# Kernel tuning notes

Hardware: AMD Instinct MI355X
Metric: run time of the kernel (lower is better)

## Reference

```python
import jax, jax.numpy as jnp
import numpy as np

B, S, D = 4, 1024, 1024
H, DK, DV = 16, 64, 64
EPS = 1e-5

def setup_inputs() -> dict:
    key = jax.random.key(0)
    ks = jax.random.split(key, 13)
    sc = lambda n: 1.0 / np.sqrt(n)
    return {
        "Q": jax.random.normal(ks[0], (B, S, D), jnp.float32),
        "K": jax.random.normal(ks[1], (B, S, D), jnp.float32),
        "V": jax.random.normal(ks[2], (B, S, D), jnp.float32),
        "Wq": jax.random.normal(ks[3], (D, H * DK), jnp.float32) * sc(D),
        "bq": jax.random.normal(ks[4], (H * DK,), jnp.float32) * 0.01,
        "Wk": jax.random.normal(ks[5], (D, H * DK), jnp.float32) * sc(D),
        "bk": jax.random.normal(ks[6], (H * DK,), jnp.float32) * 0.01,
        "Wv": jax.random.normal(ks[7], (D, H * DV), jnp.float32) * sc(D),
        "bv": jax.random.normal(ks[8], (H * DV,), jnp.float32) * 0.01,
        "Wo": jax.random.normal(ks[9], (H * DV, D), jnp.float32) * sc(H * DV),
        "bo": jax.random.normal(ks[10], (D,), jnp.float32) * 0.01,
        "pos_k": jax.random.normal(ks[11], (H * S, DK), jnp.float32) * 0.02,
        "pos_v": jax.random.normal(ks[12], (H * S, DV), jnp.float32) * 0.02,
        "gamma": jnp.ones((D,), jnp.float32),
        "beta": jnp.zeros((D,), jnp.float32),
    }

def reference(Q, K, V, Wq, bq, Wk, bk, Wv, bv, Wo, bo, pos_k, pos_v, gamma, beta):
    b = Q.shape[0]
    # projections + head split: [b, h, s, dk/dv]
    q = (Q @ Wq + bq).reshape(b, S, H, DK).transpose(0, 2, 1, 3)
    k = (K @ Wk + bk).reshape(b, S, H, DK).transpose(0, 2, 1, 3)
    v = (V @ Wv + bv).reshape(b, S, H, DV).transpose(0, 2, 1, 3)
    # pos_ids = arange(H*S).view(1, H, S) -> embedding lookup is just a reshape
    K_pos = pos_k.reshape(1, H, S, DK)
    V_pos = pos_v.reshape(1, H, S, DV)
    scores = jnp.einsum("bhqd,bhkd->bhqk", q, k + K_pos) / np.sqrt(DK).astype(np.float32)
    attn = jax.nn.softmax(scores, axis=-1)
    context = jnp.einsum("bhqk,bhkd->bhqd", attn, v + V_pos)
    context = context.transpose(0, 2, 1, 3).reshape(b, S, H * DV)
    out = context @ Wo + bo + Q  # residual
    mu = jnp.mean(out, axis=-1, keepdims=True)
    var = jnp.var(out, axis=-1, keepdims=True)
    out = (out - mu) * jax.lax.rsqrt(var + EPS) * gamma + beta
    return (out, attn)
```

## Files before the change

kernel.cpp:

```cpp
#include <hip/hip_runtime.h>
#include <cstdint>
#include <cstddef>


typedef __attribute__((ext_vector_type(8))) short short8;
typedef __attribute__((ext_vector_type(4))) short short4v;
typedef __attribute__((ext_vector_type(4))) float f32x4;

typedef __attribute__((address_space(1))) void gl_void;
typedef __attribute__((address_space(3))) void lds_void;

#define MFMA16(a, b, c) __builtin_amdgcn_mfma_f32_16x16x32_bf16(a, b, c, 0, 0, 0)
#define GLL(src, dst) __builtin_amdgcn_global_load_lds((gl_void*)(src), (lds_void*)(dst), 16, 0, 0)
#define SBAR() __builtin_amdgcn_s_barrier()
#define WAIT_VM(n) asm volatile("s_waitcnt vmcnt(" #n ")" ::: "memory")

__device__ __forceinline__ unsigned short f2bf(float f) {
  union { float f; unsigned u; } v; v.f = f;
  unsigned r = v.u + 0x7FFFu + ((v.u >> 16) & 1u);
  return (unsigned short)(r >> 16);
}
__device__ __forceinline__ float bf2f(unsigned short h) {
  union { unsigned u; float f; } v; v.u = ((unsigned)h) << 16;
  return v.f;
}

__global__ __launch_bounds__(256) void transpose_w(
    const float* __restrict__ wq, const float* __restrict__ wk,
    const float* __restrict__ wv, const float* __restrict__ wo,
    unsigned short* __restrict__ wt) {
  __shared__ unsigned short tile[64][68];
  const int z = blockIdx.z;
  const float* W = (z == 0) ? wq : (z == 1) ? wk : (z == 2) ? wv : wo;
  unsigned short* out = wt + (size_t)z * 1048576;
  const int n0 = blockIdx.x * 64, k0 = blockIdx.y * 64;
  const int tr = threadIdx.x >> 4;
  const int tc = (threadIdx.x & 15) * 4;
#pragma unroll
  for (int i = 0; i < 4; ++i) {
    int k = tr + i * 16;
    float4 x = *reinterpret_cast<const float4*>(W + (size_t)(k0 + k) * 1024 + n0 + tc);
    tile[k][tc + 0] = f2bf(x.x); tile[k][tc + 1] = f2bf(x.y);
    tile[k][tc + 2] = f2bf(x.z); tile[k][tc + 3] = f2bf(x.w);
  }
  __syncthreads();
#pragma unroll
  for (int i = 0; i < 4; ++i) {
    int n = tr + i * 16;
    short4v o;
    o[0] = (short)tile[tc + 0][n]; o[1] = (short)tile[tc + 1][n];
    o[2] = (short)tile[tc + 2][n]; o[3] = (short)tile[tc + 3][n];
    *reinterpret_cast<short4v*>(out + (size_t)(n0 + n) * 1024 + k0 + tc) = o;
  }
}

__global__ __launch_bounds__(256) void gemm_qkv(
    const float* __restrict__ Qf, const float* __restrict__ Kf,
    const float* __restrict__ Vf, const unsigned short* __restrict__ wt,
    const float* __restrict__ bq, const float* __restrict__ bk,
    const float* __restrict__ bv, const float* __restrict__ pos_k,
    const float* __restrict__ pos_v, unsigned short* __restrict__ qb,
    unsigned short* __restrict__ kbuf, unsigned short* __restrict__ vT) {
  __shared__ unsigned short lds[16384];
  const int z = blockIdx.z;
  const float* A = (z == 0) ? Qf : (z == 1) ? Kf : Vf;
  const unsigned short* Bt = wt + (size_t)z * 1048576;
  const float* bias = (z == 0) ? bq : (z == 1) ? bk : bv;

  const int tid = threadIdx.x;
  const int lane = tid & 63;
  const int w = tid >> 6;
  const int g = lane >> 4;
  const int lr = lane & 15;
  const int wg = blockIdx.y * 8 + blockIdx.x;
  const int lg = (wg & 7) * 32 + (wg >> 3);
  const int m0 = (lg >> 3) << 7;
  const int n0 = (lg & 7) << 7;
  const int wm = w >> 1, wn = w & 1;

  const int ra0 = tid >> 2, ca = tid & 3;
  const int ra1 = ra0 + 64;
  const int wA0 = ra0 * 64 + ((ca ^ ((ra0 >> 1) & 3)) << 4);
  const int wA1 = ra1 * 64 + ((ca ^ ((ra1 >> 1) & 3)) << 4);
  const float* a0p = A + (size_t)(m0 + ra0) * 1024 + ca * 8;
  const float* a1p = A + (size_t)(m0 + ra1) * 1024 + ca * 8;

  const int c0 = (w << 6) + lane;
  const int r0 = c0 >> 2;
  const int sl0 = (c0 & 3) ^ ((r0 >> 1) & 3);
  const int c1 = c0 + 256;
  const int r1 = c1 >> 2;
  const int sl1 = (c1 & 3) ^ ((r1 >> 1) & 3);
  const size_t gb0 = ((size_t)(n0 + r0) << 10) + (sl0 << 3);
  const size_t gb1 = ((size_t)(n0 + r1) << 10) + (sl1 << 3);
  char* ldsc = (char*)lds;

  int offA[4], offB[4];
#pragma unroll
  for (int i = 0; i < 4; ++i) {
    int rt = (wm << 6) + (i << 4) + lr;
    offA[i] = rt * 64 + ((g ^ ((rt >> 1) & 3)) << 4);
    int nt = (wn << 6) + (i << 4) + lr;
    offB[i] = nt * 64 + ((g ^ ((nt >> 1) & 3)) << 4);
  }

  f32x4 acc[4][4] = {};

  {
    const float4 fa = *reinterpret_cast<const float4*>(a0p);
    const float4 fb = *reinterpret_cast<const float4*>(a0p + 4);
    const float4 fc = *reinterpret_cast<const float4*>(a1p);
    const float4 fd = *reinterpret_cast<const float4*>(a1p + 4);
    short8 pa, pb;
    pa[0] = (short)f2bf(fa.x); pa[1] = (short)f2bf(fa.y);
    pa[2] = (short)f2bf(fa.z); pa[3] = (short)f2bf(fa.w);
    pa[4] = (short)f2bf(fb.x); pa[5] = (short)f2bf(fb.y);
    pa[6] = (short)f2bf(fb.z); pa[7] = (short)f2bf(fb.w);
    pb[0] = (short)f2bf(fc.x); pb[1] = (short)f2bf(fc.y);
    pb[2] = (short)f2bf(fc.z); pb[3] = (short)f2bf(fc.w);
    pb[4] = (short)f2bf(fd.x); pb[5] = (short)f2bf(fd.y);
    pb[6] = (short)f2bf(fd.z); pb[7] = (short)f2bf(fd.w);
    *reinterpret_cast<short8*>(ldsc + wA0) = pa;
    *reinterpret_cast<short8*>(ldsc + wA1) = pb;
    __builtin_amdgcn_global_load_lds((gl_void*)(Bt + gb0),
                                     (lds_void*)(ldsc + 16384 + (w << 10)), 16, 0, 0);
    __builtin_amdgcn_global_load_lds((gl_void*)(Bt + gb1),
                                     (lds_void*)(ldsc + 16384 + 4096 + (w << 10)), 16, 0, 0);
    __syncthreads();
  }

  for (int kt = 0; kt < 32; ++kt) {
    const int cur = (kt & 1) << 13;
    const int nxt = ((kt + 1) & 1) << 13;
    float4 fa, fb, fc, fd;
    if (kt < 31) {
      const int kb32 = (kt + 1) << 5;
      __builtin_amdgcn_global_load_lds((gl_void*)(Bt + gb0 + kb32),
                                       (lds_void*)(ldsc + 16384 + nxt + (w << 10)), 16, 0, 0);
      __builtin_amdgcn_global_load_lds((gl_void*)(Bt + gb1 + kb32),
                                       (lds_void*)(ldsc + 16384 + nxt + 4096 + (w << 10)), 16, 0, 0);
      fa = *reinterpret_cast<const float4*>(a0p + kb32);
      fb = *reinterpret_cast<const float4*>(a0p + kb32 + 4);
      fc = *reinterpret_cast<const float4*>(a1p + kb32);
      fd = *reinterpret_cast<const float4*>(a1p + kb32 + 4);
    }
    short8 am[4], bn[4];
#pragma unroll
    for (int i = 0; i < 4; ++i) {
      am[i] = *reinterpret_cast<const short8*>(ldsc + cur + offA[i]);
      bn[i] = *reinterpret_cast<const short8*>(ldsc + 16384 + cur + offB[i]);
    }
#pragma unroll
    for (int i = 0; i < 4; ++i)
#pragma unroll
      for (int j = 0; j < 4; ++j)
        acc[i][j] = MFMA16(am[i], bn[j], acc[i][j]);
    if (kt < 31) {
      short8 pa, pb;
      pa[0] = (short)f2bf(fa.x); pa[1] = (short)f2bf(fa.y);
      pa[2] = (short)f2bf(fa.z); pa[3] = (short)f2bf(fa.w);
      pa[4] = (short)f2bf(fb.x); pa[5] = (short)f2bf(fb.y);
      pa[6] = (short)f2bf(fb.z); pa[7] = (short)f2bf(fb.w);
      pb[0] = (short)f2bf(fc.x); pb[1] = (short)f2bf(fc.y);
      pb[2] = (short)f2bf(fc.z); pb[3] = (short)f2bf(fc.w);
      pb[4] = (short)f2bf(fd.x); pb[5] = (short)f2bf(fd.y);
      pb[6] = (short)f2bf(fd.z); pb[7] = (short)f2bf(fd.w);
      *reinterpret_cast<short8*>(ldsc + nxt + wA0) = pa;
      *reinterpret_cast<short8*>(ldsc + nxt + wA1) = pb;
    }
    __syncthreads();
  }

#pragma unroll
  for (int i = 0; i < 4; ++i) {
#pragma unroll
    for (int j = 0; j < 4; ++j) {
      const int n = n0 + (wn << 6) + (j << 4) + lr;
      const int hh = n >> 6, dk = n & 63;
      const float bs = bias[n];
      const int mb = m0 + (wm << 6) + (i << 4) + (g << 2);
      const int b = mb >> 10, s0 = mb & 1023;
      if (z == 2) {
        short4v o;
#pragma unroll
        for (int r = 0; r < 4; ++r) {
          const float val = acc[i][j][r] + bs +
                            pos_v[((((size_t)hh << 10) + s0 + r) << 6) + dk];
          o[r] = (short)f2bf(val);
        }
        *reinterpret_cast<short4v*>(
            vT + ((size_t)((b * 16 + hh) * 64 + dk) << 10) + s0) = o;
      } else {
#pragma unroll
        for (int r = 0; r < 4; ++r) {
          float val = acc[i][j][r];
          if (z == 0) {
            val = (val + bs) * 0.180336880111f;
          } else {
            val = val + bs + pos_k[((((size_t)hh << 10) + s0 + r) << 6) + dk];
          }
          unsigned short* dst = (z == 0) ? qb : kbuf;
          dst[((((size_t)(b * 16 + hh) << 10) + s0 + r) << 6) + dk] = f2bf(val);
        }
      }
    }
  }
}

__global__ __launch_bounds__(256) void attn_fused(
    const unsigned short* __restrict__ qb,
    const unsigned short* __restrict__ kb,
    const unsigned short* __restrict__ vT,
    unsigned short* __restrict__ ctxb,
    float* __restrict__ attn_out) {
  __shared__ char smem[40960];
  const int tid = threadIdx.x;
  const int lane = tid & 63;
  const int w = tid >> 6;
  const int g = lane >> 4;
  const int lr = lane & 15;
  const int wg = ((blockIdx.x & 7) << 7) + (blockIdx.x >> 3);
  const int bh = wg >> 4, qt = wg & 15;
  const int b = bh >> 4, h = bh & 15;
  const int qrow0 = (qt << 6) + (w << 4);
  const size_t headoff = (size_t)bh << 16;

  const size_t qoff = headoff + (size_t)(qrow0 + lr) * 64 + (g << 3);
  const short8 a0 = *reinterpret_cast<const short8*>(qb + qoff);
  const short8 a1 = *reinterpret_cast<const short8*>(qb + qoff + 32);

  const int key0 = tid >> 3, sl0 = (tid & 7) ^ (key0 & 7);
  const int key1 = 32 + (tid >> 3), sl1 = (tid & 7) ^ (key1 & 7);
  const unsigned short* ks0 = kb + headoff + (size_t)key0 * 64 + (sl0 << 3);
  const unsigned short* ks1 = kb + headoff + (size_t)key1 * 64 + (sl1 << 3);
  const unsigned short* vs0 = vT + headoff + ((size_t)key0 << 10) + (sl0 << 3);
  const unsigned short* vs1 = vT + headoff + ((size_t)key1 << 10) + (sl1 << 3);

  GLL(ks0, smem + (w << 10));
  GLL(ks1, smem + 4096 + (w << 10));
  GLL(ks0 + 4096, smem + 8192 + (w << 10));
  GLL(ks1 + 4096, smem + 8192 + 4096 + (w << 10));

  float l[4] = {0.f, 0.f, 0.f, 0.f};
  for (int ct = 0; ct < 16; ++ct) {
    if (ct < 15) WAIT_VM(2); else WAIT_VM(0);
    SBAR();
    const char* kl = smem + ((ct & 1) << 13);
#pragma unroll
    for (int kf = 0; kf < 4; ++kf) {
      const int kr = (kf << 4) + lr;
      const char* row = kl + (kr << 7);
      const short8 b0 = *reinterpret_cast<const short8*>(row + ((g ^ (kr & 7)) << 4));
      const short8 b1 = *reinterpret_cast<const short8*>(row + (((4 + g) ^ (kr & 7)) << 4));
      f32x4 acc = {0.f, 0.f, 0.f, 0.f};
      acc = MFMA16(a0, b0, acc);
      acc = MFMA16(a1, b1, acc);
#pragma unroll
      for (int r = 0; r < 4; ++r) l[r] += exp2f(acc[r]);
    }
    SBAR();
    if (ct + 2 < 16) {
      const int koff = (ct + 2) << 12;
      const int bo = (ct & 1) << 13;
      GLL(ks0 + koff, smem + bo + (w << 10));
      GLL(ks1 + koff, smem + bo + 4096 + (w << 10));
    }
  }
#pragma unroll
  for (int r = 0; r < 4; ++r) {
    l[r] += __shfl_xor(l[r], 1);
    l[r] += __shfl_xor(l[r], 2);
    l[r] += __shfl_xor(l[r], 4);
    l[r] += __shfl_xor(l[r], 8);
  }
  float inv[4];
#pragma unroll
  for (int r = 0; r < 4; ++r) inv[r] = 1.0f / l[r];

  GLL(ks0, smem + (w << 10));
  GLL(ks1, smem + 4096 + (w << 10));
  GLL(vs0, smem + 16384 + (w << 10));
  GLL(vs1, smem + 16384 + 4096 + (w << 10));
  GLL(ks0 + 4096, smem + 8192 + (w << 10));
  GLL(ks1 + 4096, smem + 8192 + 4096 + (w << 10));
  GLL(vs0 + 64, smem + 16384 + 8192 + (w << 10));
  GLL(vs1 + 64, smem + 16384 + 8192 + 4096 + (w << 10));

  char* ew = smem + 32768 + (w << 11);
  float* ab = attn_out + ((size_t)bh << 20);
  f32x4 ctx[4] = {};

  for (int ct = 0; ct < 16; ++ct) {
    if (ct == 0) { WAIT_VM(4); }
    else if (ct == 15) { WAIT_VM(4); }
    else { WAIT_VM(8); }
    SBAR();
    const int cur = (ct & 1) << 13;
    const int kc0 = ct << 6;
    const char* kl = smem + cur;
    const char* vl = smem + 16384 + cur;

#pragma unroll
    for (int kf = 0; kf < 4; ++kf) {
      const int kr = (kf << 4) + lr;
      const char* row = kl + (kr << 7);
      const short8 b0 = *reinterpret_cast<const short8*>(row + ((g ^ (kr & 7)) << 4));
      const short8 b1 = *reinterpret_cast<const short8*>(row + (((4 + g) ^ (kr & 7)) << 4));
      f32x4 acc = {0.f, 0.f, 0.f, 0.f};
      acc = MFMA16(a0, b0, acc);
      acc = MFMA16(a1, b1, acc);
#pragma unroll
      for (int r = 0; r < 4; ++r) {
        const float p = exp2f(acc[r]) * inv[r];
        const int prow = (g << 2) + r;
        const int kc = (kf << 4) + lr;
        *(unsigned short*)(ew + (prow << 7) + ((((kc >> 3) ^ (prow & 7))) << 4) +
                           ((kc & 7) << 1)) = f2bf(p);
      }
    }

#pragma unroll
    for (int p2 = 0; p2 < 2; ++p2) {
      const int row = lane >> 2;
      const int s = (lane & 3) + (p2 << 2);
      const short8 pv = *reinterpret_cast<const short8*>(
          ew + (row << 7) + ((s ^ (row & 7)) << 4));
      float* dst = ab + ((size_t)(qrow0 + row) << 10) + kc0 + (s << 3);
      float4 o0, o1;
      o0.x = bf2f((unsigned short)pv[0]); o0.y = bf2f((unsigned short)pv[1]);
      o0.z = bf2f((unsigned short)pv[2]); o0.w = bf2f((unsigned short)pv[3]);
      o1.x = bf2f((unsigned short)pv[4]); o1.y = bf2f((unsigned short)pv[5]);
      o1.z = bf2f((unsigned short)pv[6]); o1.w = bf2f((unsigned short)pv[7]);
      *reinterpret_cast<float4*>(dst) = o0;
      *reinterpret_cast<float4*>(dst + 4) = o1;
    }

    const short8 pa0 = *reinterpret_cast<const short8*>(
        ew + (lr << 7) + ((g ^ (lr & 7)) << 4));
    const short8 pa1 = *reinterpret_cast<const short8*>(
        ew + (lr << 7) + (((4 + g) ^ (lr & 7)) << 4));
#pragma unroll
    for (int dt = 0; dt < 4; ++dt) {
      const int dv = (dt << 4) + lr;
      const char* vrow = vl + (dv << 7);
      const short8 v0 = *reinterpret_cast<const short8*>(vrow + ((g ^ (dv & 7)) << 4));
      const short8 v1 = *reinterpret_cast<const short8*>(vrow + (((4 + g) ^ (dv & 7)) << 4));
      ctx[dt] = MFMA16(pa0, v0, ctx[dt]);
      ctx[dt] = MFMA16(pa1, v1, ctx[dt]);
    }
    SBAR();
    if (ct + 2 < 16) {
      const int kn = (ct + 2) << 6;
      const int bo = (ct & 1) << 13;
      GLL(ks0 + ((size_t)kn << 6), smem + bo + (w << 10));
      GLL(ks1 + ((size_t)kn << 6), smem + bo + 4096 + (w << 10));
      GLL(vs0 + kn, smem + 16384 + bo + (w << 10));
      GLL(vs1 + kn, smem + 16384 + bo + 4096 + (w << 10));
    }
  }

#pragma unroll
  for (int dt = 0; dt < 4; ++dt) {
#pragma unroll
    for (int r = 0; r < 4; ++r) {
      const int srow = qrow0 + (g << 2) + r;
      const int n = (h << 6) + (dt << 4) + lr;
      ctxb[((((size_t)(b << 10)) + srow) << 10) + n] = f2bf(ctx[dt][r]);
    }
  }
}

__global__ __launch_bounds__(256) void gemm_out(
    const unsigned short* __restrict__ A, const unsigned short* __restrict__ Bt,
    const float* __restrict__ bias, const float* __restrict__ resid,
    float* __restrict__ outf) {
  __shared__ unsigned short lds[16384];
  const int tid = threadIdx.x;
  const int lane = tid & 63;
  const int w = tid >> 6;
  const int g = lane >> 4;
  const int lr = lane & 15;
  const int wg = blockIdx.y * 8 + blockIdx.x;
  const int lg = (wg & 7) * 32 + (wg >> 3);
  const int m0 = (lg >> 3) << 7;
  const int n0 = (lg & 7) << 7;
  const int wm = w >> 1, wn = w & 1;

  const int c0 = (w << 6) + lane;
  const int r0 = c0 >> 2;
  const int sl0 = (c0 & 3) ^ ((r0 >> 1) & 3);
  const int c1 = c0 + 256;
  const int r1 = c1 >> 2;
  const int sl1 = (c1 & 3) ^ ((r1 >> 1) & 3);

  const size_t ga0 = ((size_t)(m0 + r0) << 10) + (sl0 << 3);
  const size_t ga1 = ((size_t)(m0 + r1) << 10) + (sl1 << 3);
  const size_t gb0 = ((size_t)(n0 + r0) << 10) + (sl0 << 3);
  const size_t gb1 = ((size_t)(n0 + r1) << 10) + (sl1 << 3);

  char* ldsc = (char*)lds;

  int offA[4], offB[4];
#pragma unroll
  for (int i = 0; i < 4; ++i) {
    int rt = (wm << 6) + (i << 4) + lr;
    offA[i] = rt * 64 + ((g ^ ((rt >> 1) & 3)) << 4);
    int nt = (wn << 6) + (i << 4) + lr;
    offB[i] = nt * 64 + ((g ^ ((nt >> 1) & 3)) << 4);
  }

  __builtin_amdgcn_global_load_lds((gl_void*)(A + ga0),
                                   (lds_void*)(ldsc + (w << 10)), 16, 0, 0);
  __builtin_amdgcn_global_load_lds((gl_void*)(A + ga1),
                                   (lds_void*)(ldsc + 4096 + (w << 10)), 16, 0, 0);
  __builtin_amdgcn_global_load_lds((gl_void*)(Bt + gb0),
                                   (lds_void*)(ldsc + 16384 + (w << 10)), 16, 0, 0);
  __builtin_amdgcn_global_load_lds((gl_void*)(Bt + gb1),
                                   (lds_void*)(ldsc + 16384 + 4096 + (w << 10)), 16, 0, 0);
  __syncthreads();

  f32x4 acc[4][4] = {};
  for (int kt = 0; kt < 32; ++kt) {
    const int cur = (kt & 1) << 13;
    if (kt < 31) {
      const int nxt = ((kt + 1) & 1) << 13;
      const int kb32 = (kt + 1) << 5;
      __builtin_amdgcn_global_load_lds((gl_void*)(A + ga0 + kb32),
                                       (lds_void*)(ldsc + nxt + (w << 10)), 16, 0, 0);
      __builtin_amdgcn_global_load_lds((gl_void*)(A + ga1 + kb32),
                                       (lds_void*)(ldsc + nxt + 4096 + (w << 10)), 16, 0, 0);
      __builtin_amdgcn_global_load_lds((gl_void*)(Bt + gb0 + kb32),
                                       (lds_void*)(ldsc + 16384 + nxt + (w << 10)), 16, 0, 0);
      __builtin_amdgcn_global_load_lds((gl_void*)(Bt + gb1 + kb32),
                                       (lds_void*)(ldsc + 16384 + nxt + 4096 + (w << 10)), 16, 0, 0);
    }
    short8 am[4], bn[4];
#pragma unroll
    for (int i = 0; i < 4; ++i) {
      am[i] = *reinterpret_cast<const short8*>(ldsc + cur + offA[i]);
      bn[i] = *reinterpret_cast<const short8*>(ldsc + 16384 + cur + offB[i]);
    }
#pragma unroll
    for (int i = 0; i < 4; ++i)
#pragma unroll
      for (int j = 0; j < 4; ++j)
        acc[i][j] = MFMA16(am[i], bn[j], acc[i][j]);
    __syncthreads();
  }

#pragma unroll
  for (int i = 0; i < 4; ++i) {
#pragma unroll
    for (int j = 0; j < 4; ++j) {
      const int n = n0 + (wn << 6) + (j << 4) + lr;
      const float bs = bias[n];
#pragma unroll
      for (int r = 0; r < 4; ++r) {
        const int m = m0 + (wm << 6) + (i << 4) + (g << 2) + r;
        outf[((size_t)m << 10) + n] =
            acc[i][j][r] + bs + resid[((size_t)m << 10) + n];
      }
    }
  }
}

__global__ __launch_bounds__(256) void layernorm_kernel(
    const float* __restrict__ x, const float* __restrict__ gamma,
    const float* __restrict__ beta, float* __restrict__ out) {
  __shared__ float red[8];
  const int row = blockIdx.x, t = threadIdx.x;
  const float4 v = *reinterpret_cast<const float4*>(x + ((size_t)row << 10) + t * 4);
  float s1 = v.x + v.y + v.z + v.w;
  float s2 = v.x * v.x + v.y * v.y + v.z * v.z + v.w * v.w;
#pragma unroll
  for (int off = 1; off < 64; off <<= 1) {
    s1 += __shfl_xor(s1, off);
    s2 += __shfl_xor(s2, off);
  }
  const int w = t >> 6;
  if ((t & 63) == 0) { red[w * 2] = s1; red[w * 2 + 1] = s2; }
  __syncthreads();
  s1 = red[0] + red[2] + red[4] + red[6];
  s2 = red[1] + red[3] + red[5] + red[7];
  const float mu = s1 * (1.0f / 1024.0f);
  const float var = s2 * (1.0f / 1024.0f) - mu * mu;
  const float rs = rsqrtf(var + 1e-5f);
  const float4 gm = *reinterpret_cast<const float4*>(gamma + t * 4);
  const float4 bt = *reinterpret_cast<const float4*>(beta + t * 4);
  float4 o;
  o.x = (v.x - mu) * rs * gm.x + bt.x;
  o.y = (v.y - mu) * rs * gm.y + bt.y;
  o.z = (v.z - mu) * rs * gm.z + bt.z;
  o.w = (v.w - mu) * rs * gm.w + bt.w;
  *reinterpret_cast<float4*>(out + ((size_t)row << 10) + t * 4) = o;
}

static constexpr size_t OFF_QB = 0;
static constexpr size_t OFF_KB = 8388608;
static constexpr size_t OFF_VT = 16777216;
static constexpr size_t OFF_WT = 25165824;
static constexpr size_t OFF_CTX = 33554432;
static constexpr size_t OFF_LN = 41943040;

extern "C" void kernel_launch(void* const* d_in, const int* in_sizes, int n_in,
                              void* d_out, int out_size, void* d_ws, size_t ws_size,
                              hipStream_t stream) {
  (void)in_sizes; (void)n_in; (void)out_size; (void)ws_size;
  const float* Q = (const float*)d_in[0];
  const float* K = (const float*)d_in[1];
  const float* V = (const float*)d_in[2];
  const float* Wq = (const float*)d_in[3];
  const float* bq = (const float*)d_in[4];
  const float* Wk = (const float*)d_in[5];
  const float* bk = (const float*)d_in[6];
  const float* Wv = (const float*)d_in[7];
  const float* bv = (const float*)d_in[8];
  const float* Wo = (const float*)d_in[9];
  const float* bo = (const float*)d_in[10];
  const float* pos_k = (const float*)d_in[11];
  const float* pos_v = (const float*)d_in[12];
  const float* gamma = (const float*)d_in[13];
  const float* beta = (const float*)d_in[14];

  char* ws = (char*)d_ws;
  unsigned short* qb = (unsigned short*)(ws + OFF_QB);
  unsigned short* kb = (unsigned short*)(ws + OFF_KB);
  unsigned short* vT = (unsigned short*)(ws + OFF_VT);
  unsigned short* wt = (unsigned short*)(ws + OFF_WT);
  unsigned short* ctxb = (unsigned short*)(ws + OFF_CTX);
  float* lnb = (float*)(ws + OFF_LN);

  float* outF = (float*)d_out;
  float* attnF = outF + 4194304;

  transpose_w<<<dim3(16, 16, 4), 256, 0, stream>>>(Wq, Wk, Wv, Wo, wt);
  gemm_qkv<<<dim3(8, 32, 3), 256, 0, stream>>>(Q, K, V, wt, bq, bk, bv,
                                               pos_k, pos_v, qb, kb, vT);
  attn_fused<<<dim3(1024), 256, 0, stream>>>(qb, kb, vT, ctxb, attnF);
  gemm_out<<<dim3(8, 32), 256, 0, stream>>>(ctxb, wt + 3145728, bo, Q, lnb);
  layernorm_kernel<<<4096, 256, 0, stream>>>(lnb, gamma, beta, outF);
}
```

Baseline: 198.4 us.

## Double attention block size to 128 queries and pipeline gemm_out loads two stages ahead

The attention kernel now runs 512 threads per block covering 128 query rows, so each K/V tile staged in LDS is reused by eight waves instead of four. With eight waves, each thread issues one tile load instead of two, and the LDS footprint grows to make room for the extra per-wave softmax scratch. Separately, gemm_out switches from one-step prefetch with __syncthreads to a two-deep global_load_lds pipeline with explicit vmcnt waits and barriers. Risks are lower occupancy and fewer blocks per CU for attention, and a correctness dependency on the hand-counted vmcnt values.

```diff
diff --git a/kernel.cpp b/kernel.cpp
--- a/kernel.cpp
+++ b/kernel.cpp
@@ -207,22 +207,22 @@
   }
 }
 
-__global__ __launch_bounds__(256) void attn_fused(
+__global__ __launch_bounds__(512) void attn_fused(
     const unsigned short* __restrict__ qb,
     const unsigned short* __restrict__ kb,
     const unsigned short* __restrict__ vT,
     unsigned short* __restrict__ ctxb,
     float* __restrict__ attn_out) {
-  __shared__ char smem[40960];
+  __shared__ char smem[49152];
   const int tid = threadIdx.x;
   const int lane = tid & 63;
   const int w = tid >> 6;
   const int g = lane >> 4;
   const int lr = lane & 15;
-  const int wg = ((blockIdx.x & 7) << 7) + (blockIdx.x >> 3);
-  const int bh = wg >> 4, qt = wg & 15;
+  const int wg = ((blockIdx.x & 7) << 6) + (blockIdx.x >> 3);
+  const int bh = wg >> 3, qt = wg & 7;
   const int b = bh >> 4, h = bh & 15;
-  const int qrow0 = (qt << 6) + (w << 4);
+  const int qrow0 = (qt << 7) + (w << 4);
   const size_t headoff = (size_t)bh << 16;
 
   const size_t qoff = headoff + (size_t)(qrow0 + lr) * 64 + (g << 3);
@@ -230,20 +230,15 @@
   const short8 a1 = *reinterpret_cast<const short8*>(qb + qoff + 32);
 
   const int key0 = tid >> 3, sl0 = (tid & 7) ^ (key0 & 7);
-  const int key1 = 32 + (tid >> 3), sl1 = (tid & 7) ^ (key1 & 7);
   const unsigned short* ks0 = kb + headoff + (size_t)key0 * 64 + (sl0 << 3);
-  const unsigned short* ks1 = kb + headoff + (size_t)key1 * 64 + (sl1 << 3);
   const unsigned short* vs0 = vT + headoff + ((size_t)key0 << 10) + (sl0 << 3);
-  const unsigned short* vs1 = vT + headoff + ((size_t)key1 << 10) + (sl1 << 3);
 
   GLL(ks0, smem + (w << 10));
-  GLL(ks1, smem + 4096 + (w << 10));
   GLL(ks0 + 4096, smem + 8192 + (w << 10));
-  GLL(ks1 + 4096, smem + 8192 + 4096 + (w << 10));
 
   float l[4] = {0.f, 0.f, 0.f, 0.f};
   for (int ct = 0; ct < 16; ++ct) {
-    if (ct < 15) WAIT_VM(2); else WAIT_VM(0);
+    if (ct < 15) WAIT_VM(1); else WAIT_VM(0);
     SBAR();
     const char* kl = smem + ((ct & 1) << 13);
 #pragma unroll
@@ -260,10 +255,7 @@
     }
     SBAR();
     if (ct + 2 < 16) {
-      const int koff = (ct + 2) << 12;
-      const int bo = (ct & 1) << 13;
-      GLL(ks0 + koff, smem + bo + (w << 10));
-      GLL(ks1 + koff, smem + bo + 4096 + (w << 10));
+      GLL(ks0 + ((ct + 2) << 12), smem + ((ct & 1) << 13) + (w << 10));
     }
   }
 #pragma unroll
@@ -278,22 +270,16 @@
   for (int r = 0; r < 4; ++r) inv[r] = 1.0f / l[r];
 
   GLL(ks0, smem + (w << 10));
-  GLL(ks1, smem + 4096 + (w << 10));
   GLL(vs0, smem + 16384 + (w << 10));
-  GLL(vs1, smem + 16384 + 4096 + (w << 10));
   GLL(ks0 + 4096, smem + 8192 + (w << 10));
-  GLL(ks1 + 4096, smem + 8192 + 4096 + (w << 10));
   GLL(vs0 + 64, smem + 16384 + 8192 + (w << 10));
-  GLL(vs1 + 64, smem + 16384 + 8192 + 4096 + (w << 10));
 
   char* ew = smem + 32768 + (w << 11);
   float* ab = attn_out + ((size_t)bh << 20);
   f32x4 ctx[4] = {};
 
   for (int ct = 0; ct < 16; ++ct) {
-    if (ct == 0) { WAIT_VM(4); }
-    else if (ct == 15) { WAIT_VM(4); }
-    else { WAIT_VM(8); }
+    if (ct == 0 || ct == 15) { WAIT_VM(2); } else { WAIT_VM(4); }
     SBAR();
     const int cur = (ct & 1) << 13;
     const int kc0 = ct << 6;
@@ -353,9 +339,7 @@
       const int kn = (ct + 2) << 6;
       const int bo = (ct & 1) << 13;
       GLL(ks0 + ((size_t)kn << 6), smem + bo + (w << 10));
-      GLL(ks1 + ((size_t)kn << 6), smem + bo + 4096 + (w << 10));
       GLL(vs0 + kn, smem + 16384 + bo + (w << 10));
-      GLL(vs1 + kn, smem + 16384 + bo + 4096 + (w << 10));
     }
   }
 
@@ -409,31 +393,20 @@
     offB[i] = nt * 64 + ((g ^ ((nt >> 1) & 3)) << 4);
   }
 
-  __builtin_amdgcn_global_load_lds((gl_void*)(A + ga0),
-                                   (lds_void*)(ldsc + (w << 10)), 16, 0, 0);
-  __builtin_amdgcn_global_load_lds((gl_void*)(A + ga1),
-                                   (lds_void*)(ldsc + 4096 + (w << 10)), 16, 0, 0);
-  __builtin_amdgcn_global_load_lds((gl_void*)(Bt + gb0),
-                                   (lds_void*)(ldsc + 16384 + (w << 10)), 16, 0, 0);
-  __builtin_amdgcn_global_load_lds((gl_void*)(Bt + gb1),
-                                   (lds_void*)(ldsc + 16384 + 4096 + (w << 10)), 16, 0, 0);
-  __syncthreads();
+  GLL(A + ga0, ldsc + (w << 10));
+  GLL(A + ga1, ldsc + 4096 + (w << 10));
+  GLL(Bt + gb0, ldsc + 16384 + (w << 10));
+  GLL(Bt + gb1, ldsc + 16384 + 4096 + (w << 10));
+  GLL(A + ga0 + 32, ldsc + 8192 + (w << 10));
+  GLL(A + ga1 + 32, ldsc + 8192 + 4096 + (w << 10));
+  GLL(Bt + gb0 + 32, ldsc + 16384 + 8192 + (w << 10));
+  GLL(Bt + gb1 + 32, ldsc + 16384 + 8192 + 4096 + (w << 10));
 
   f32x4 acc[4][4] = {};
   for (int kt = 0; kt < 32; ++kt) {
+    if (kt < 31) WAIT_VM(4); else WAIT_VM(0);
+    SBAR();
     const int cur = (kt & 1) << 13;
-    if (kt < 31) {
-      const int nxt = ((kt + 1) & 1) << 13;
-      const int kb32 = (kt + 1) << 5;
-      __builtin_amdgcn_global_load_lds((gl_void*)(A + ga0 + kb32),
-                                       (lds_void*)(ldsc + nxt + (w << 10)), 16, 0, 0);
-      __builtin_amdgcn_global_load_lds((gl_void*)(A + ga1 + kb32),
-                                       (lds_void*)(ldsc + nxt + 4096 + (w << 10)), 16, 0, 0);
-      __builtin_amdgcn_global_load_lds((gl_void*)(Bt + gb0 + kb32),
-                                       (lds_void*)(ldsc + 16384 + nxt + (w << 10)), 16, 0, 0);
-      __builtin_amdgcn_global_load_lds((gl_void*)(Bt + gb1 + kb32),
-                                       (lds_void*)(ldsc + 16384 + nxt + 4096 + (w << 10)), 16, 0, 0);
-    }
     short8 am[4], bn[4];
 #pragma unroll
     for (int i = 0; i < 4; ++i) {
@@ -445,7 +418,14 @@
 #pragma unroll
       for (int j = 0; j < 4; ++j)
         acc[i][j] = MFMA16(am[i], bn[j], acc[i][j]);
-    __syncthreads();
+    SBAR();
+    if (kt < 30) {
+      const int kb32 = (kt + 2) << 5;
+      GLL(A + ga0 + kb32, ldsc + cur + (w << 10));
+      GLL(A + ga1 + kb32, ldsc + cur + 4096 + (w << 10));
+      GLL(Bt + gb0 + kb32, ldsc + 16384 + cur + (w << 10));
+      GLL(Bt + gb1 + kb32, ldsc + 16384 + cur + 4096 + (w << 10));
+    }
   }
 
 #pragma unroll
@@ -536,7 +516,7 @@
   transpose_w<<<dim3(16, 16, 4), 256, 0, stream>>>(Wq, Wk, Wv, Wo, wt);
   gemm_qkv<<<dim3(8, 32, 3), 256, 0, stream>>>(Q, K, V, wt, bq, bk, bv,
                                                pos_k, pos_v, qb, kb, vT);
-  attn_fused<<<dim3(1024), 256, 0, stream>>>(qb, kb, vT, ctxb, attnF);
+  attn_fused<<<dim3(512), 512, 0, stream>>>(qb, kb, vT, ctxb, attnF);
   gemm_out<<<dim3(8, 32), 256, 0, stream>>>(ctxb, wt + 3145728, bo, Q, lnb);
   layernorm_kernel<<<4096, 256, 0, stream>>>(lnb, gamma, beta, outF);
 }
```

New measurement: 212.3 us. 7.0% more time.

## Store V in MFMA-fragment packed layout and read it directly from global

Applied to the files above, without the earlier changes.

The QKV projection now writes V in a packed layout where each group of 8 keys for a given dv is contiguous, matching the B-operand fragment of the bf16 MFMA. The attention kernel then loads V fragments straight from global memory instead of staging them through LDS with global_load_lds. This drops the V double buffer, shrinking shared memory from 40KB to 24KB to allow more resident blocks, and removes LDS traffic for V. The trade-off is exposed global or L2 latency inside the PV loop, plus re-tuned vmcnt wait counts that must stay correct alongside the other outstanding loads and stores.

```diff
diff --git a/kernel.cpp b/kernel.cpp
--- a/kernel.cpp
+++ b/kernel.cpp
@@ -60,7 +60,7 @@
     const float* __restrict__ bq, const float* __restrict__ bk,
     const float* __restrict__ bv, const float* __restrict__ pos_k,
     const float* __restrict__ pos_v, unsigned short* __restrict__ qb,
-    unsigned short* __restrict__ kbuf, unsigned short* __restrict__ vT) {
+    unsigned short* __restrict__ kbuf, unsigned short* __restrict__ vP) {
   __shared__ unsigned short lds[16384];
   const int z = blockIdx.z;
   const float* A = (z == 0) ? Qf : (z == 1) ? Kf : Vf;
@@ -189,7 +189,8 @@
           o[r] = (short)f2bf(val);
         }
         *reinterpret_cast<short4v*>(
-            vT + ((size_t)((b * 16 + hh) * 64 + dk) << 10) + s0) = o;
+            vP + ((size_t)(b * 16 + hh) << 16) + ((s0 >> 3) << 9) + (dk << 3) +
+            (s0 & 7)) = o;
       } else {
 #pragma unroll
         for (int r = 0; r < 4; ++r) {
@@ -210,10 +211,10 @@
 __global__ __launch_bounds__(256) void attn_fused(
     const unsigned short* __restrict__ qb,
     const unsigned short* __restrict__ kb,
-    const unsigned short* __restrict__ vT,
+    const unsigned short* __restrict__ vP,
     unsigned short* __restrict__ ctxb,
     float* __restrict__ attn_out) {
-  __shared__ char smem[40960];
+  __shared__ char smem[24576];
   const int tid = threadIdx.x;
   const int lane = tid & 63;
   const int w = tid >> 6;
@@ -233,8 +234,6 @@
   const int key1 = 32 + (tid >> 3), sl1 = (tid & 7) ^ (key1 & 7);
   const unsigned short* ks0 = kb + headoff + (size_t)key0 * 64 + (sl0 << 3);
   const unsigned short* ks1 = kb + headoff + (size_t)key1 * 64 + (sl1 << 3);
-  const unsigned short* vs0 = vT + headoff + ((size_t)key0 << 10) + (sl0 << 3);
-  const unsigned short* vs1 = vT + headoff + ((size_t)key1 << 10) + (sl1 << 3);
 
   GLL(ks0, smem + (w << 10));
   GLL(ks1, smem + 4096 + (w << 10));
@@ -243,7 +242,7 @@
 
   float l[4] = {0.f, 0.f, 0.f, 0.f};
   for (int ct = 0; ct < 16; ++ct) {
-    if (ct < 15) WAIT_VM(2); else WAIT_VM(0);
+    if (ct < 15) { WAIT_VM(2); } else { WAIT_VM(0); }
     SBAR();
     const char* kl = smem + ((ct & 1) << 13);
 #pragma unroll
@@ -279,26 +278,21 @@
 
   GLL(ks0, smem + (w << 10));
   GLL(ks1, smem + 4096 + (w << 10));
-  GLL(vs0, smem + 16384 + (w << 10));
-  GLL(vs1, smem + 16384 + 4096 + (w << 10));
   GLL(ks0 + 4096, smem + 8192 + (w << 10));
   GLL(ks1 + 4096, smem + 8192 + 4096 + (w << 10));
-  GLL(vs0 + 64, smem + 16384 + 8192 + (w << 10));
-  GLL(vs1 + 64, smem + 16384 + 8192 + 4096 + (w << 10));
-
-  char* ew = smem + 32768 + (w << 11);
+
+  char* ew = smem + 16384 + (w << 11);
   float* ab = attn_out + ((size_t)bh << 20);
   f32x4 ctx[4] = {};
 
   for (int ct = 0; ct < 16; ++ct) {
-    if (ct == 0) { WAIT_VM(4); }
-    else if (ct == 15) { WAIT_VM(4); }
-    else { WAIT_VM(8); }
+    if (ct == 0) { WAIT_VM(2); }
+    else if (ct == 15) { WAIT_VM(10); }
+    else { WAIT_VM(12); }
     SBAR();
     const int cur = (ct & 1) << 13;
     const int kc0 = ct << 6;
     const char* kl = smem + cur;
-    const char* vl = smem + 16384 + cur;
 
 #pragma unroll
     for (int kf = 0; kf < 4; ++kf) {
@@ -339,12 +333,13 @@
         ew + (lr << 7) + ((g ^ (lr & 7)) << 4));
     const short8 pa1 = *reinterpret_cast<const short8*>(
         ew + (lr << 7) + (((4 + g) ^ (lr & 7)) << 4));
+    const unsigned short* vch0 = vP + headoff + ((size_t)((kc0 >> 3) + g) << 9);
+    const unsigned short* vch1 = vch0 + (4 << 9);
 #pragma unroll
     for (int dt = 0; dt < 4; ++dt) {
       const int dv = (dt << 4) + lr;
-      const char* vrow = vl + (dv << 7);
-      const short8 v0 = *reinterpret_cast<const short8*>(vrow + ((g ^ (dv & 7)) << 4));
-      const short8 v1 = *reinterpret_cast<const short8*>(vrow + (((4 + g) ^ (dv & 7)) << 4));
+      const short8 v0 = *reinterpret_cast<const short8*>(vch0 + (dv << 3));
+      const short8 v1 = *reinterpret_cast<const short8*>(vch1 + (dv << 3));
       ctx[dt] = MFMA16(pa0, v0, ctx[dt]);
       ctx[dt] = MFMA16(pa1, v1, ctx[dt]);
     }
@@ -354,8 +349,6 @@
       const int bo = (ct & 1) << 13;
       GLL(ks0 + ((size_t)kn << 6), smem + bo + (w << 10));
       GLL(ks1 + ((size_t)kn << 6), smem + bo + 4096 + (w << 10));
-      GLL(vs0 + kn, smem + 16384 + bo + (w << 10));
-      GLL(vs1 + kn, smem + 16384 + bo + 4096 + (w << 10));
     }
   }
 
@@ -497,7 +490,7 @@
 
 static constexpr size_t OFF_QB = 0;
 static constexpr size_t OFF_KB = 8388608;
-static constexpr size_t OFF_VT = 16777216;
+static constexpr size_t OFF_VP = 16777216;
 static constexpr size_t OFF_WT = 25165824;
 static constexpr size_t OFF_CTX = 33554432;
 static constexpr size_t OFF_LN = 41943040;
@@ -525,7 +518,7 @@
   char* ws = (char*)d_ws;
   unsigned short* qb = (unsigned short*)(ws + OFF_QB);
   unsigned short* kb = (unsigned short*)(ws + OFF_KB);
-  unsigned short* vT = (unsigned short*)(ws + OFF_VT);
+  unsigned short* vP = (unsigned short*)(ws + OFF_VP);
   unsigned short* wt = (unsigned short*)(ws + OFF_WT);
   unsigned short* ctxb = (unsigned short*)(ws + OFF_CTX);
   float* lnb = (float*)(ws + OFF_LN);
@@ -535,8 +528,8 @@
 
   transpose_w<<<dim3(16, 16, 4), 256, 0, stream>>>(Wq, Wk, Wv, Wo, wt);
   gemm_qkv<<<dim3(8, 32, 3), 256, 0, stream>>>(Q, K, V, wt, bq, bk, bv,
-                                               pos_k, pos_v, qb, kb, vT);
-  attn_fused<<<dim3(1024), 256, 0, stream>>>(qb, kb, vT, ctxb, attnF);
+                                               pos_k, pos_v, qb, kb, vP);
+  attn_fused<<<dim3(1024), 256, 0, stream>>>(qb, kb, vP, ctxb, attnF);
   gemm_out<<<dim3(8, 32), 256, 0, stream>>>(ctxb, wt + 3145728, bo, Q, lnb);
   layernorm_kernel<<<4096, 256, 0, stream>>>(lnb, gamma, beta, outF);
 }
```

After: 194.8 us. About the same (-1.8%).
